# Optimization experiments

Measured on AMD Instinct MI355X. Metric: run time of the kernel, lower is better.

## Reference

```python
import jax, jax.numpy as jnp
import numpy as np

NDIM = 1024
NHEAD = 16
B, T = 4, 2048
EPS = 1e-05
GELU_C = np.sqrt(2.0 / np.pi).astype(np.float32)


def new_gelu(x):
    return 0.5 * x * (1.0 + jnp.tanh(GELU_C * (x + 0.044715 * x ** 3)))


def layer_norm(x, w, b):
    mu = jnp.mean(x, axis=-1, keepdims=True)
    var = jnp.var(x, axis=-1, keepdims=True)
    return (x - mu) * jax.lax.rsqrt(var + EPS) * w + b


def setup_inputs() -> dict:
    key = jax.random.key(0)
    ks = jax.random.split(key, 8)
    d, dff = NDIM, 4 * NDIM
    s = 0.02
    return {
        "x": jax.random.normal(ks[0], (B, T, d), jnp.float32),
        "ln1_w": jnp.ones((d,), jnp.float32),
        "ln1_b": jnp.zeros((d,), jnp.float32),
        "w_attn": jax.random.normal(ks[1], (d, 3 * d), jnp.float32) * s,
        "b_attn": jnp.zeros((3 * d,), jnp.float32),
        "w_proj": jax.random.normal(ks[2], (d, d), jnp.float32) * s,
        "b_proj": jnp.zeros((d,), jnp.float32),
        "ln2_w": jnp.ones((d,), jnp.float32),
        "ln2_b": jnp.zeros((d,), jnp.float32),
        "w_fc": jax.random.normal(ks[3], (d, dff), jnp.float32) * s,
        "b_fc": jnp.zeros((dff,), jnp.float32),
        "w_fc2": jax.random.normal(ks[4], (dff, d), jnp.float32) * s,
        "b_fc2": jnp.zeros((d,), jnp.float32),
    }


def reference(x, ln1_w, ln1_b, w_attn, b_attn, w_proj, b_proj,
              ln2_w, ln2_b, w_fc, b_fc, w_fc2, b_fc2):
    Bx, Tx, C = x.shape
    hd = C // NHEAD
    # --- attention ---
    h = layer_norm(x, ln1_w, ln1_b)
    qkv = h @ w_attn + b_attn                       # [B,T,3C]
    q, k, v = jnp.split(qkv, 3, axis=-1)
    q = q.reshape(Bx, Tx, NHEAD, hd).transpose(0, 2, 1, 3)  # [B,H,T,hd]
    k = k.reshape(Bx, Tx, NHEAD, hd).transpose(0, 2, 1, 3)
    v = v.reshape(Bx, Tx, NHEAD, hd).transpose(0, 2, 1, 3)
    att = jnp.einsum('bhqd,bhkd->bhqk', q, k) * (1.0 / np.sqrt(hd).astype(np.float32))
    causal = jnp.tril(jnp.ones((Tx, Tx), bool))
    att = jnp.where(causal[None, None], att, jnp.float32(-jnp.inf))
    att = jax.nn.softmax(att, axis=-1)
    y = jnp.einsum('bhqk,bhkd->bhqd', att, v)
    y = y.transpose(0, 2, 1, 3).reshape(Bx, Tx, C)
    x = x + y @ w_proj + b_proj
    # --- MLP ---
    h2 = layer_norm(x, ln2_w, ln2_b)
    x = x + new_gelu(h2 @ w_fc + b_fc) @ w_fc2 + b_fc2
    return x
```

## Files before the change

kernel.cpp:

```cpp
#include <hip/hip_runtime.h>

typedef __attribute__((ext_vector_type(8))) short short8;
typedef __attribute__((ext_vector_type(8))) unsigned short ushort8;
typedef __attribute__((ext_vector_type(4))) float f32x4;
typedef __attribute__((ext_vector_type(16))) float f32x16;
typedef __attribute__((ext_vector_type(2))) unsigned int uint2v;
typedef unsigned int uint32;

__device__ __forceinline__ unsigned short f2bf(float f){
  union { float f; unsigned int u; } x; x.f = f;
  unsigned int u = x.u;
  u += 0x7fffu + ((u >> 16) & 1u);
  return (unsigned short)(u >> 16);
}
__device__ __forceinline__ float bf2f(unsigned short s){
  union { float f; unsigned int u; } x; x.u = ((uint32)s) << 16; return x.f;
}

typedef __attribute__((address_space(1))) void gvoid;
typedef __attribute__((address_space(3))) void lvoid;
__device__ __forceinline__ void gload_lds16(const void* g, void* l){
  __builtin_amdgcn_global_load_lds((gvoid*)g, (lvoid*)l, 16, 0, 0);
}

__device__ __forceinline__ f32x4 mfma_bf16(short8 a, short8 b, f32x4 c){
  return __builtin_amdgcn_mfma_f32_16x16x32_bf16(a, b, c, 0, 0, 0);
}
__device__ __forceinline__ f32x16 mfma32(short8 a, short8 b, f32x16 c){
  return __builtin_amdgcn_mfma_f32_32x32x16_bf16(a, b, c, 0, 0, 0);
}

__device__ __forceinline__ uint32 cvtpk_bf(float lo, float hi){
  uint32 r;
  asm("v_cvt_pk_bf16_f32 %0, %1, %2" : "=v"(r) : "v"(lo), "v"(hi));
  return r;
}
__device__ __forceinline__ void plswap(uint32& a, uint32& b){
  auto r = __builtin_amdgcn_permlane32_swap(a, b, false, false);
  a = r[0]; b = r[1];
}

#if __has_builtin(__builtin_amdgcn_exp2f)
__device__ __forceinline__ float exp2g(float x){ return __builtin_amdgcn_exp2f(x); }
#else
__device__ __forceinline__ float exp2g(float x){ return exp2f(x); }
#endif
#if __has_builtin(__builtin_amdgcn_rcpf)
__device__ __forceinline__ float rcpg(float x){ return __builtin_amdgcn_rcpf(x); }
#else
__device__ __forceinline__ float rcpg(float x){ return 1.0f / x; }
#endif

__device__ __forceinline__ float gelu_fast(float v){
  const float u = 0.7978845608028654f * (v + 0.044715f * v * v * v);
  const float E = exp2g(2.8853900817779268f * u);
  return v - v * rcpg(1.0f + E);
}

__device__ __forceinline__ f32x16 zero16(){
  f32x16 z;
  #pragma unroll
  for (int i = 0; i < 16; i++) z[i] = 0.0f;
  return z;
}

__global__ __launch_bounds__(256) void wtrans_all_kernel(
    const float* __restrict__ w0, unsigned short* __restrict__ t0,
    const float* __restrict__ w1, unsigned short* __restrict__ t1,
    const float* __restrict__ w2, unsigned short* __restrict__ t2,
    const float* __restrict__ w3, unsigned short* __restrict__ t3)
{
  __shared__ float tile[32][33];
  const int bt = blockIdx.x;
  const float* w; unsigned short* wt; int K, N, ti;
  if (bt < 3072)      { w = w0; wt = t0; K = 1024; N = 3072; ti = bt; }
  else if (bt < 4096) { w = w1; wt = t1; K = 1024; N = 1024; ti = bt - 3072; }
  else if (bt < 8192) { w = w2; wt = t2; K = 1024; N = 4096; ti = bt - 4096; }
  else                { w = w3; wt = t3; K = 4096; N = 1024; ti = bt - 8192; }
  const int nbx = N >> 5;
  const int n0 = (ti % nbx) << 5;
  const int k0 = (ti / nbx) << 5;
  const int t = threadIdx.x;
  #pragma unroll
  for (int i = 0; i < 4; i++){
    const int e = t + i * 256;
    const int r = e >> 5, c = e & 31;
    tile[r][c] = w[(size_t)(k0 + r) * N + n0 + c];
  }
  __syncthreads();
  #pragma unroll
  for (int i = 0; i < 4; i++){
    const int e = t + i * 256;
    const int r = e >> 5, c = e & 31;
    wt[(size_t)(n0 + r) * K + k0 + c] = f2bf(tile[c][r]);
  }
}

__global__ __launch_bounds__(256) void vtrans_kernel(
    const unsigned short* __restrict__ qkv, unsigned short* __restrict__ vt)
{
  __shared__ unsigned short tile[32][33];
  const int bh = blockIdx.z;
  const int b = bh >> 4, h = bh & 15;
  const int t0 = blockIdx.x * 32;
  const int f0 = blockIdx.y * 32;
  const int t = threadIdx.x;
  #pragma unroll
  for (int i = 0; i < 4; i++){
    const int e = t + i * 256;
    const int r = e >> 5, c = e & 31;
    tile[r][c] = qkv[(size_t)(b * 2048 + t0 + r) * 3072 + 2048 + h * 64 + f0 + c];
  }
  __syncthreads();
  #pragma unroll
  for (int i = 0; i < 4; i++){
    const int e = t + i * 256;
    const int r = e >> 5, c = e & 31;
    vt[((size_t)bh * 64 + f0 + r) * 2048 + t0 + c] = tile[c][r];
  }
}

__global__ __launch_bounds__(256) void ln_kernel(
    const float* __restrict__ x, const float* __restrict__ w, const float* __restrict__ b,
    unsigned short* __restrict__ out)
{
  const int row = blockIdx.x;
  const int t = threadIdx.x;
  const float4 v = ((const float4*)(x + (size_t)row * 1024))[t];
  float s  = v.x + v.y + v.z + v.w;
  float s2 = v.x * v.x + v.y * v.y + v.z * v.z + v.w * v.w;
  #pragma unroll
  for (int off = 32; off > 0; off >>= 1){
    s  += __shfl_xor(s, off);
    s2 += __shfl_xor(s2, off);
  }
  __shared__ float ps[8];
  const int wid = t >> 6;
  if ((t & 63) == 0){ ps[wid] = s; ps[4 + wid] = s2; }
  __syncthreads();
  s  = ps[0] + ps[1] + ps[2] + ps[3];
  s2 = ps[4] + ps[5] + ps[6] + ps[7];
  const float mu  = s * (1.0f / 1024.0f);
  const float var = s2 * (1.0f / 1024.0f) - mu * mu;
  const float rs  = rsqrtf(var + 1e-5f);
  const float4 wv = ((const float4*)w)[t];
  const float4 bv = ((const float4*)b)[t];
  ushort4 ov;
  ov.x = f2bf((v.x - mu) * rs * wv.x + bv.x);
  ov.y = f2bf((v.y - mu) * rs * wv.y + bv.y);
  ov.z = f2bf((v.z - mu) * rs * wv.z + bv.z);
  ov.w = f2bf((v.w - mu) * rs * wv.w + bv.w);
  ((ushort4*)(out + (size_t)row * 1024))[t] = ov;
}

__global__ __launch_bounds__(256) void ln_bf16_kernel(
    const unsigned short* __restrict__ x, const float* __restrict__ w,
    const float* __restrict__ b, unsigned short* __restrict__ out)
{
  const int row = blockIdx.x;
  const int t = threadIdx.x;
  const ushort4 raw = ((const ushort4*)(x + (size_t)row * 1024))[t];
  const float v0 = bf2f(raw.x), v1 = bf2f(raw.y), v2 = bf2f(raw.z), v3 = bf2f(raw.w);
  float s  = v0 + v1 + v2 + v3;
  float s2 = v0 * v0 + v1 * v1 + v2 * v2 + v3 * v3;
  #pragma unroll
  for (int off = 32; off > 0; off >>= 1){
    s  += __shfl_xor(s, off);
    s2 += __shfl_xor(s2, off);
  }
  __shared__ float ps[8];
  const int wid = t >> 6;
  if ((t & 63) == 0){ ps[wid] = s; ps[4 + wid] = s2; }
  __syncthreads();
  s  = ps[0] + ps[1] + ps[2] + ps[3];
  s2 = ps[4] + ps[5] + ps[6] + ps[7];
  const float mu  = s * (1.0f / 1024.0f);
  const float var = s2 * (1.0f / 1024.0f) - mu * mu;
  const float rs  = rsqrtf(var + 1e-5f);
  const float4 wv = ((const float4*)w)[t];
  const float4 bv = ((const float4*)b)[t];
  ushort4 ov;
  ov.x = f2bf((v0 - mu) * rs * wv.x + bv.x);
  ov.y = f2bf((v1 - mu) * rs * wv.y + bv.y);
  ov.z = f2bf((v2 - mu) * rs * wv.z + bv.z);
  ov.w = f2bf((v3 - mu) * rs * wv.w + bv.w);
  ((ushort4*)(out + (size_t)row * 1024))[t] = ov;
}

#define EPI_BF16        0
#define EPI_GELU        1
#define EPI_RESF_OBF    2
#define EPI_RESBF_OF32  3

template<int EPI>
__device__ __forceinline__ void epi_store(void* outp, const void* res,
                                          size_t idx, float v){
  if (EPI == EPI_RESF_OBF){
    ((unsigned short*)outp)[idx] = f2bf(v + ((const float*)res)[idx]);
  } else if (EPI == EPI_RESBF_OF32){
    ((float*)outp)[idx] = v + bf2f(((const unsigned short*)res)[idx]);
  } else if (EPI == EPI_GELU){
    ((unsigned short*)outp)[idx] = f2bf(gelu_fast(v));
  } else {
    ((unsigned short*)outp)[idx] = f2bf(v);
  }
}

template<int EPI>
__global__ __launch_bounds__(256, 2) void gemm5_kernel(
    const unsigned short* __restrict__ A,
    const unsigned short* __restrict__ BT,
    const float* __restrict__ bias,
    const void* __restrict__ res,
    void* __restrict__ outp,
    int M, int N, int K)
{
  constexpr int SLOT = 24576;
  __shared__ __align__(16) char lds[3 * SLOT];

  const int nwg = gridDim.x;
  const int bid = blockIdx.x;
  const int wg = (bid & 7) * (nwg >> 3) + (bid >> 3);
  const int NT = N >> 8;
  const int mt = wg / NT;
  const int nti = wg - mt * NT;
  const int m0 = mt << 7;
  const int n0 = nti << 8;

  const int tid = threadIdx.x;
  const int lane = tid & 63;
  const int wid = tid >> 6;
  const int fr = lane & 15;
  const int fg = lane >> 4;

  const unsigned short* aSrc[2]; int aDst[2];
  #pragma unroll
  for (int l = 0; l < 2; l++){
    const int s = l * 256 + tid;
    const int r = s >> 2, c = s & 3;
    aSrc[l] = A + (size_t)(m0 + r) * K + ((c ^ ((r >> 1) & 3)) << 3);
    aDst[l] = s * 16;
  }
  const unsigned short* bSrc[4]; int bDst[4];
  #pragma unroll
  for (int l = 0; l < 4; l++){
    const int s = l * 256 + tid;
    const int r = s >> 2, c = s & 3;
    bSrc[l] = BT + (size_t)(n0 + r) * K + ((c ^ ((r >> 1) & 3)) << 3);
    bDst[l] = 8192 + s * 16;
  }

  int aOff[8], bOff[4];
  #pragma unroll
  for (int mi = 0; mi < 8; mi++){
    const int row = mi * 16 + fr;
    aOff[mi] = row * 64 + ((fg ^ ((row >> 1) & 3)) << 4);
  }
  #pragma unroll
  for (int nj = 0; nj < 4; nj++){
    const int row = wid * 64 + nj * 16 + fr;
    bOff[nj] = 8192 + row * 64 + ((fg ^ ((row >> 1) & 3)) << 4);
  }

  f32x4 acc[8][4];
  #pragma unroll
  for (int i = 0; i < 8; i++)
    #pragma unroll
    for (int j = 0; j < 4; j++) acc[i][j] = (f32x4){0.f, 0.f, 0.f, 0.f};

#define STAGE5(sl, slot) do { \
    gload_lds16(aSrc[0] + (size_t)(sl) * 32, lds + (slot) + aDst[0]); \
    gload_lds16(aSrc[1] + (size_t)(sl) * 32, lds + (slot) + aDst[1]); \
    gload_lds16(bSrc[0] + (size_t)(sl) * 32, lds + (slot) + bDst[0]); \
    gload_lds16(bSrc[1] + (size_t)(sl) * 32, lds + (slot) + bDst[1]); \
    gload_lds16(bSrc[2] + (size_t)(sl) * 32, lds + (slot) + bDst[2]); \
    gload_lds16(bSrc[3] + (size_t)(sl) * 32, lds + (slot) + bDst[3]); \
  } while (0)

  const int NS = K >> 5;

  STAGE5(0, 0);
  STAGE5(1, SLOT);
  asm volatile("s_waitcnt vmcnt(6)" ::: "memory");
  __builtin_amdgcn_s_barrier();
  asm volatile("" ::: "memory");

  int cs = 0, cg = 2 * SLOT;
  for (int s = 0; s < NS; s++){
    short8 aF[8], bF[4];
    #pragma unroll
    for (int mi = 0; mi < 8; mi++)
      aF[mi] = *(const short8*)(lds + cs + aOff[mi]);
    #pragma unroll
    for (int nj = 0; nj < 4; nj++)
      bF[nj] = *(const short8*)(lds + cs + bOff[nj]);
    if (s + 2 < NS) STAGE5(s + 2, cg);
    #pragma unroll
    for (int mi = 0; mi < 8; mi++)
      #pragma unroll
      for (int nj = 0; nj < 4; nj++)
        acc[mi][nj] = mfma_bf16(aF[mi], bF[nj], acc[mi][nj]);

    if (s + 2 < NS){
      asm volatile("s_waitcnt vmcnt(6)" ::: "memory");
    } else if (s + 1 < NS){
      asm volatile("s_waitcnt vmcnt(0)" ::: "memory");
    }
    __builtin_amdgcn_s_barrier();
    asm volatile("" ::: "memory");

    cs += SLOT; if (cs == 3 * SLOT) cs = 0;
    cg += SLOT; if (cg == 3 * SLOT) cg = 0;
  }
#undef STAGE5

  #pragma unroll
  for (int mi = 0; mi < 8; mi++){
    const int mrow = m0 + mi * 16 + fg * 4;
    #pragma unroll
    for (int nj = 0; nj < 4; nj++){
      const int ncol = n0 + wid * 64 + nj * 16 + fr;
      const float bv = bias[ncol];
      #pragma unroll
      for (int r2 = 0; r2 < 4; r2++){
        const size_t idx = (size_t)(mrow + r2) * N + ncol;
        epi_store<EPI>(outp, res, idx, acc[mi][nj][r2] + bv);
      }
    }
  }
}

template<int EPI>
__global__ __launch_bounds__(256, 3) void gemm7_kernel(
    const unsigned short* __restrict__ A,
    const unsigned short* __restrict__ BT,
    const float* __restrict__ bias,
    const void* __restrict__ res,
    void* __restrict__ outp,
    int M, int N, int K)
{
  constexpr int SLOT = 16384;
  __shared__ __align__(16) char lds[3 * SLOT];

  const int nwg = gridDim.x;
  const int bid = blockIdx.x;
  const int wg = (bid & 7) * (nwg >> 3) + (bid >> 3);
  const int NT = N >> 7;
  const int mt = wg / NT;
  const int nti = wg - mt * NT;
  const int m0 = mt << 7;
  const int n0 = nti << 7;

  const int tid = threadIdx.x;
  const int lane = tid & 63;
  const int wid = tid >> 6;
  const int wv_m = wid >> 1;
  const int wv_n = wid & 1;
  const int fr = lane & 15;
  const int fg = lane >> 4;

  const unsigned short* aSrc[2]; int aDst[2];
  const unsigned short* bSrc[2]; int bDst[2];
  #pragma unroll
  for (int l = 0; l < 2; l++){
    const int s = l * 256 + tid;
    const int r = s >> 2, c = s & 3;
    const int co = (c ^ ((r >> 1) & 3)) << 3;
    aSrc[l] = A  + (size_t)(m0 + r) * K + co;
    bSrc[l] = BT + (size_t)(n0 + r) * K + co;
    aDst[l] = s * 16;
    bDst[l] = 8192 + s * 16;
  }

  int aOff[4], bOff[4];
  #pragma unroll
  for (int mi = 0; mi < 4; mi++){
    const int row = wv_m * 64 + mi * 16 + fr;
    aOff[mi] = row * 64 + ((fg ^ ((row >> 1) & 3)) << 4);
  }
  #pragma unroll
  for (int nj = 0; nj < 4; nj++){
    const int row = wv_n * 64 + nj * 16 + fr;
    bOff[nj] = 8192 + row * 64 + ((fg ^ ((row >> 1) & 3)) << 4);
  }

  f32x4 acc[4][4];
  #pragma unroll
  for (int i = 0; i < 4; i++)
    #pragma unroll
    for (int j = 0; j < 4; j++) acc[i][j] = (f32x4){0.f, 0.f, 0.f, 0.f};

#define STAGE7(sl, slot) do { \
    gload_lds16(aSrc[0] + (size_t)(sl) * 32, lds + (slot) + aDst[0]); \
    gload_lds16(aSrc[1] + (size_t)(sl) * 32, lds + (slot) + aDst[1]); \
    gload_lds16(bSrc[0] + (size_t)(sl) * 32, lds + (slot) + bDst[0]); \
    gload_lds16(bSrc[1] + (size_t)(sl) * 32, lds + (slot) + bDst[1]); \
  } while (0)

  const int NS = K >> 5;

  STAGE7(0, 0);
  STAGE7(1, SLOT);
  asm volatile("s_waitcnt vmcnt(4)" ::: "memory");
  __builtin_amdgcn_s_barrier();
  asm volatile("" ::: "memory");

  int cs = 0, cg = 2 * SLOT;
  for (int s = 0; s < NS; s++){
    short8 aF[4], bF[4];
    #pragma unroll
    for (int mi = 0; mi < 4; mi++)
      aF[mi] = *(const short8*)(lds + cs + aOff[mi]);
    #pragma unroll
    for (int nj = 0; nj < 4; nj++)
      bF[nj] = *(const short8*)(lds + cs + bOff[nj]);
    if (s + 2 < NS) STAGE7(s + 2, cg);
    #pragma unroll
    for (int mi = 0; mi < 4; mi++)
      #pragma unroll
      for (int nj = 0; nj < 4; nj++)
        acc[mi][nj] = mfma_bf16(aF[mi], bF[nj], acc[mi][nj]);

    if (s + 2 < NS){
      asm volatile("s_waitcnt vmcnt(4)" ::: "memory");
    } else if (s + 1 < NS){
      asm volatile("s_waitcnt vmcnt(0)" ::: "memory");
    }
    __builtin_amdgcn_s_barrier();
    asm volatile("" ::: "memory");

    cs += SLOT; if (cs == 3 * SLOT) cs = 0;
    cg += SLOT; if (cg == 3 * SLOT) cg = 0;
  }
#undef STAGE7

  #pragma unroll
  for (int mi = 0; mi < 4; mi++){
    const int mrow = m0 + wv_m * 64 + mi * 16 + fg * 4;
    #pragma unroll
    for (int nj = 0; nj < 4; nj++){
      const int ncol = n0 + wv_n * 64 + nj * 16 + fr;
      const float bv = bias[ncol];
      #pragma unroll
      for (int r2 = 0; r2 < 4; r2++){
        const size_t idx = (size_t)(mrow + r2) * N + ncol;
        epi_store<EPI>(outp, res, idx, acc[mi][nj][r2] + bv);
      }
    }
  }
}

template<bool MASK>
__device__ __forceinline__ void attn_tile(
    const unsigned short* __restrict__ Kc, const unsigned short* __restrict__ Vc,
    const short8 (&qf)[4], int kvbase, int qg, int l31, int hi,
    float& m_r, float& lsum, f32x16& Oa, f32x16& Ob)
{
  f32x16 Sa = zero16();
  f32x16 Sb = zero16();
  const int xb = l31 & 7;
  #pragma unroll
  for (int kk = 0; kk < 4; kk++){
    const int x = kk * 2 + hi;
    const short8 k0 = *(const short8*)((const char*)Kc + l31 * 128 + ((x ^ xb) << 4));
    const short8 k1 = *(const short8*)((const char*)Kc + (l31 + 32) * 128 + ((x ^ xb) << 4));
    Sa = mfma32(k0, qf[kk], Sa);
    Sb = mfma32(k1, qf[kk], Sb);
  }
  if (MASK){
    #pragma unroll
    for (int r = 0; r < 16; r++){
      const int kva = kvbase + (r & 3) + 8 * (r >> 2) + 4 * hi;
      Sa[r] = (kva > qg)      ? -1e30f : Sa[r];
      Sb[r] = (kva + 32 > qg) ? -1e30f : Sb[r];
    }
  }
  float tmax = Sa[0];
  #pragma unroll
  for (int r = 1; r < 16; r++) tmax = fmaxf(tmax, Sa[r]);
  #pragma unroll
  for (int r = 0; r < 16; r++) tmax = fmaxf(tmax, Sb[r]);
  tmax = fmaxf(tmax, __shfl_xor(tmax, 32));
  if (__any(tmax > m_r + 10.0f)){
    const float mn = fmaxf(m_r, tmax);
    const float sc = exp2g(m_r - mn);
    m_r = mn;
    lsum *= sc;
    #pragma unroll
    for (int r = 0; r < 16; r++){ Oa[r] *= sc; Ob[r] *= sc; }
  }
  float rs = 0.0f;
  #pragma unroll
  for (int r = 0; r < 16; r++){
    Sa[r] = exp2g(Sa[r] - m_r); rs += Sa[r];
    Sb[r] = exp2g(Sb[r] - m_r); rs += Sb[r];
  }
  rs += __shfl_xor(rs, 32);
  lsum += rs;

  short8 pf[4];
  {
    uint32 a0 = cvtpk_bf(Sa[0], Sa[1]),   b0 = cvtpk_bf(Sa[4], Sa[5]);
    uint32 a1 = cvtpk_bf(Sa[2], Sa[3]),   b1 = cvtpk_bf(Sa[6], Sa[7]);
    plswap(a0, b0); plswap(a1, b1);
    uint32 a2 = cvtpk_bf(Sa[8], Sa[9]),   b2 = cvtpk_bf(Sa[12], Sa[13]);
    uint32 a3 = cvtpk_bf(Sa[10], Sa[11]), b3 = cvtpk_bf(Sa[14], Sa[15]);
    plswap(a2, b2); plswap(a3, b3);
    union { uint32 u[4]; short8 s; } m0, m1;
    m0.u[0] = a0; m0.u[1] = a1; m0.u[2] = b0; m0.u[3] = b1;
    m1.u[0] = a2; m1.u[1] = a3; m1.u[2] = b2; m1.u[3] = b3;
    pf[0] = m0.s; pf[1] = m1.s;
  }
  {
    uint32 a0 = cvtpk_bf(Sb[0], Sb[1]),   b0 = cvtpk_bf(Sb[4], Sb[5]);
    uint32 a1 = cvtpk_bf(Sb[2], Sb[3]),   b1 = cvtpk_bf(Sb[6], Sb[7]);
    plswap(a0, b0); plswap(a1, b1);
    uint32 a2 = cvtpk_bf(Sb[8], Sb[9]),   b2 = cvtpk_bf(Sb[12], Sb[13]);
    uint32 a3 = cvtpk_bf(Sb[10], Sb[11]), b3 = cvtpk_bf(Sb[14], Sb[15]);
    plswap(a2, b2); plswap(a3, b3);
    union { uint32 u[4]; short8 s; } m0, m1;
    m0.u[0] = a0; m0.u[1] = a1; m0.u[2] = b0; m0.u[3] = b1;
    m1.u[0] = a2; m1.u[1] = a3; m1.u[2] = b2; m1.u[3] = b3;
    pf[2] = m0.s; pf[3] = m1.s;
  }
  #pragma unroll
  for (int kk = 0; kk < 4; kk++){
    const int x = kk * 2 + hi;
    const short8 v0 = *(const short8*)((const char*)Vc + l31 * 128 + ((x ^ xb) << 4));
    const short8 v1 = *(const short8*)((const char*)Vc + (l31 + 32) * 128 + ((x ^ xb) << 4));
    Oa = mfma32(v0, pf[kk], Oa);
    Ob = mfma32(v1, pf[kk], Ob);
  }
}

__global__ __launch_bounds__(256) void attn_kernel(
    const unsigned short* __restrict__ qkv,
    const unsigned short* __restrict__ vt,
    unsigned short* __restrict__ y)
{
  __shared__ __align__(16) unsigned short Klds[2][4096];
  __shared__ __align__(16) unsigned short Vlds[2][4096];
  const int bid = blockIdx.x;
  const int bh = bid & 63;
  const int qb_i = 15 - (bid >> 6);
  const int b = bh >> 4, h = bh & 15;
  const int qb0 = qb_i * 128;
  const int tid = threadIdx.x;
  const int w = tid >> 6;
  const int lane = tid & 63;
  const int l31 = lane & 31;
  const int hi = lane >> 5;

  const int qrow_g = b * 2048 + qb0 + w * 32 + l31;
  const unsigned short* qp = qkv + (size_t)qrow_g * 3072 + h * 64;
  short8 qf[4];
  #pragma unroll
  for (int kk = 0; kk < 4; kk++){
    short8 raw = *(const short8*)&qp[kk * 16 + hi * 8];
    #pragma unroll
    for (int j = 0; j < 8; j++)
      qf[kk][j] = (short)f2bf(bf2f((unsigned short)raw[j]) * 0.18033688011112042f);
  }

  const int sr = tid >> 3;
  const int ce = ((tid & 7) ^ (sr & 7)) * 8;
  const unsigned short* kb = qkv + (size_t)(b * 2048) * 3072 + 1024 + h * 64;
  const unsigned short* vb = vt + (size_t)bh * 64 * 2048;

  f32x16 Oa = zero16(), Ob = zero16();
  float m_r = -1e30f, lsum = 0.0f;
  const int qmin = qb0 + w * 32;
  const int qmax = qmin + 31;
  const int qg = qmin + l31;
  const int nkv = (qb0 >> 6) + 2;

#define STAGE(t, bb) do { \
    const size_t kro = (size_t)((t) * 64 + sr) * 3072; \
    gload_lds16(kb + kro + ce,                         (char*)&Klds[bb][0] + tid * 16); \
    gload_lds16(kb + kro + (size_t)32 * 3072 + ce,     (char*)&Klds[bb][0] + 4096 + tid * 16); \
    gload_lds16(vb + (size_t)sr * 2048 + (t) * 64 + ce,        (char*)&Vlds[bb][0] + tid * 16); \
    gload_lds16(vb + (size_t)(sr + 32) * 2048 + (t) * 64 + ce, (char*)&Vlds[bb][0] + 4096 + tid * 16); \
  } while (0)

  STAGE(0, 0);
  __syncthreads();
  int cur = 0;
  for (int kvt = 0; kvt < nkv; kvt++){
    if (kvt + 1 < nkv){
      if (cur) STAGE(kvt + 1, 0); else STAGE(kvt + 1, 1);
    }
    if (kvt * 64 <= qmax){
      if (kvt * 64 + 63 <= qmin)
        attn_tile<false>(Klds[cur], Vlds[cur], qf, kvt * 64, qg, l31, hi, m_r, lsum, Oa, Ob);
      else
        attn_tile<true >(Klds[cur], Vlds[cur], qf, kvt * 64, qg, l31, hi, m_r, lsum, Oa, Ob);
    }
    __syncthreads();
    cur ^= 1;
  }
#undef STAGE

  const float inv = 1.0f / lsum;
  unsigned short* yp = y + (size_t)qrow_g * 1024 + h * 64;
  #pragma unroll
  for (int c2 = 0; c2 < 4; c2++){
    uint2v da, db;
    da.x = cvtpk_bf(Oa[4 * c2 + 0] * inv, Oa[4 * c2 + 1] * inv);
    da.y = cvtpk_bf(Oa[4 * c2 + 2] * inv, Oa[4 * c2 + 3] * inv);
    *(uint2v*)&yp[8 * c2 + 4 * hi] = da;
    db.x = cvtpk_bf(Ob[4 * c2 + 0] * inv, Ob[4 * c2 + 1] * inv);
    db.y = cvtpk_bf(Ob[4 * c2 + 2] * inv, Ob[4 * c2 + 3] * inv);
    *(uint2v*)&yp[32 + 8 * c2 + 4 * hi] = db;
  }
}

extern "C" void kernel_launch(void* const* d_in, const int* in_sizes, int n_in,
                              void* d_out, int out_size, void* d_ws, size_t ws_size,
                              hipStream_t stream)
{
  const float* x      = (const float*)d_in[0];
  const float* ln1_w  = (const float*)d_in[1];
  const float* ln1_b  = (const float*)d_in[2];
  const float* w_attn = (const float*)d_in[3];
  const float* b_attn = (const float*)d_in[4];
  const float* w_proj = (const float*)d_in[5];
  const float* b_proj = (const float*)d_in[6];
  const float* ln2_w  = (const float*)d_in[7];
  const float* ln2_b  = (const float*)d_in[8];
  const float* w_fc   = (const float*)d_in[9];
  const float* b_fc   = (const float*)d_in[10];
  const float* w_fc2  = (const float*)d_in[11];
  const float* b_fc2  = (const float*)d_in[12];

  char* ws = (char*)d_ws;
  unsigned short* wbT_attn = (unsigned short*)(ws + 0);
  unsigned short* wbT_proj = (unsigned short*)(ws + 6291456);
  unsigned short* wbT_fc   = (unsigned short*)(ws + 8388608);
  unsigned short* wbT_fc2  = (unsigned short*)(ws + 16777216);
  unsigned short* h_bf     = (unsigned short*)(ws + 25165824);
  unsigned short* qkv_bf   = (unsigned short*)(ws + 41943040);
  unsigned short* vt_bf    = (unsigned short*)(ws + 92274688);
  unsigned short* g_bf     = (unsigned short*)(ws + 41943040);
  unsigned short* y_bf     = (unsigned short*)(ws + 109051904);
  unsigned short* x1_bf    = (unsigned short*)(ws + 125829120);
  float* outf = (float*)d_out;

  wtrans_all_kernel<<<12288, 256, 0, stream>>>(
      w_attn, wbT_attn, w_proj, wbT_proj, w_fc, wbT_fc, w_fc2, wbT_fc2);

  ln_kernel<<<8192, 256, 0, stream>>>(x, ln1_w, ln1_b, h_bf);
  gemm5_kernel<EPI_BF16><<<768, 256, 0, stream>>>(
      h_bf, wbT_attn, b_attn, nullptr, qkv_bf, 8192, 3072, 1024);
  vtrans_kernel<<<dim3(64, 2, 64), 256, 0, stream>>>(qkv_bf, vt_bf);
  attn_kernel<<<1024, 256, 0, stream>>>(qkv_bf, vt_bf, y_bf);
  gemm7_kernel<EPI_RESF_OBF><<<512, 256, 0, stream>>>(
      y_bf, wbT_proj, b_proj, x, x1_bf, 8192, 1024, 1024);
  ln_bf16_kernel<<<8192, 256, 0, stream>>>(x1_bf, ln2_w, ln2_b, h_bf);
  gemm5_kernel<EPI_GELU><<<1024, 256, 0, stream>>>(
      h_bf, wbT_fc, b_fc, nullptr, g_bf, 8192, 4096, 1024);
  gemm7_kernel<EPI_RESBF_OF32><<<512, 256, 0, stream>>>(
      g_bf, wbT_fc2, b_fc2, x1_bf, outf, 8192, 1024, 4096);
}
```

Baseline: 343.8 us.

## Split-K the fc2 GEMM with 128x256 tiles and a separate reduction kernel

The final fc2 GEMM (K=4096) now runs on the larger 128x256 gemm5 tile path with K split into two halves. Each half writes a bf16 partial into reused scratch buffers (h_bf, y_bf). A new row-wise kernel then sums the two partials, adds the bias and the x1 residual, and writes fp32 output. The aim is more work per workgroup and better tile efficiency while keeping 512 workgroups in flight. In exchange it adds an extra kernel launch, extra global traffic for the partials, and precision loss from rounding the partials to bf16.

```diff
diff --git a/kernel.cpp b/kernel.cpp
--- a/kernel.cpp
+++ b/kernel.cpp
@@ -187,10 +187,31 @@
   ((ushort4*)(out + (size_t)row * 1024))[t] = ov;
 }
 
+__global__ __launch_bounds__(256) void skred_kernel(
+    const unsigned short* __restrict__ p0, const unsigned short* __restrict__ p1,
+    const float* __restrict__ bias, const unsigned short* __restrict__ x1,
+    float* __restrict__ out)
+{
+  const int row = blockIdx.x;
+  const int t = threadIdx.x;
+  const size_t base = (size_t)row * 1024 + t * 4;
+  const ushort4 a = *(const ushort4*)(p0 + base);
+  const ushort4 b = *(const ushort4*)(p1 + base);
+  const ushort4 c = *(const ushort4*)(x1 + base);
+  const float4 bv = ((const float4*)bias)[t];
+  float4 o;
+  o.x = bf2f(a.x) + bf2f(b.x) + bv.x + bf2f(c.x);
+  o.y = bf2f(a.y) + bf2f(b.y) + bv.y + bf2f(c.y);
+  o.z = bf2f(a.z) + bf2f(b.z) + bv.z + bf2f(c.z);
+  o.w = bf2f(a.w) + bf2f(b.w) + bv.w + bf2f(c.w);
+  *(float4*)(out + base) = o;
+}
+
 #define EPI_BF16        0
 #define EPI_GELU        1
 #define EPI_RESF_OBF    2
 #define EPI_RESBF_OF32  3
+#define EPI_PARTBF      4
 
 template<int EPI>
 __device__ __forceinline__ void epi_store(void* outp, const void* res,
@@ -207,25 +228,15 @@
 }
 
 template<int EPI>
-__global__ __launch_bounds__(256, 2) void gemm5_kernel(
+__device__ __forceinline__ void gemm5_core(
     const unsigned short* __restrict__ A,
     const unsigned short* __restrict__ BT,
     const float* __restrict__ bias,
     const void* __restrict__ res,
     void* __restrict__ outp,
-    int M, int N, int K)
+    int N, int K, int Ks, int m0, int n0, char* lds)
 {
   constexpr int SLOT = 24576;
-  __shared__ __align__(16) char lds[3 * SLOT];
-
-  const int nwg = gridDim.x;
-  const int bid = blockIdx.x;
-  const int wg = (bid & 7) * (nwg >> 3) + (bid >> 3);
-  const int NT = N >> 8;
-  const int mt = wg / NT;
-  const int nti = wg - mt * NT;
-  const int m0 = mt << 7;
-  const int n0 = nti << 8;
 
   const int tid = threadIdx.x;
   const int lane = tid & 63;
@@ -238,7 +249,7 @@
   for (int l = 0; l < 2; l++){
     const int s = l * 256 + tid;
     const int r = s >> 2, c = s & 3;
-    aSrc[l] = A + (size_t)(m0 + r) * K + ((c ^ ((r >> 1) & 3)) << 3);
+    aSrc[l] = A + (size_t)(m0 + r) * Ks + ((c ^ ((r >> 1) & 3)) << 3);
     aDst[l] = s * 16;
   }
   const unsigned short* bSrc[4]; int bDst[4];
@@ -246,7 +257,7 @@
   for (int l = 0; l < 4; l++){
     const int s = l * 256 + tid;
     const int r = s >> 2, c = s & 3;
-    bSrc[l] = BT + (size_t)(n0 + r) * K + ((c ^ ((r >> 1) & 3)) << 3);
+    bSrc[l] = BT + (size_t)(n0 + r) * Ks + ((c ^ ((r >> 1) & 3)) << 3);
     bDst[l] = 8192 + s * 16;
   }
 
@@ -320,7 +331,7 @@
     #pragma unroll
     for (int nj = 0; nj < 4; nj++){
       const int ncol = n0 + wid * 64 + nj * 16 + fr;
-      const float bv = bias[ncol];
+      const float bv = (EPI == EPI_PARTBF) ? 0.0f : bias[ncol];
       #pragma unroll
       for (int r2 = 0; r2 < 4; r2++){
         const size_t idx = (size_t)(mrow + r2) * N + ncol;
@@ -328,6 +339,48 @@
       }
     }
   }
+}
+
+template<int EPI>
+__global__ __launch_bounds__(256, 2) void gemm5_kernel(
+    const unsigned short* __restrict__ A,
+    const unsigned short* __restrict__ BT,
+    const float* __restrict__ bias,
+    const void* __restrict__ res,
+    void* __restrict__ outp,
+    int M, int N, int K)
+{
+  __shared__ __align__(16) char lds[3 * 24576];
+  const int nwg = gridDim.x;
+  const int bid = blockIdx.x;
+  const int wg = (bid & 7) * (nwg >> 3) + (bid >> 3);
+  const int NT = N >> 8;
+  const int mt = wg / NT;
+  const int nti = wg - mt * NT;
+  gemm5_core<EPI>(A, BT, bias, res, outp, N, K, K, mt << 7, nti << 8, lds);
+}
+
+__global__ __launch_bounds__(256, 2) void gemm5sk_kernel(
+    const unsigned short* __restrict__ A,
+    const unsigned short* __restrict__ BT,
+    unsigned short* __restrict__ p0,
+    unsigned short* __restrict__ p1,
+    int N, int Khalf, int Ks)
+{
+  __shared__ __align__(16) char lds[3 * 24576];
+  const int nwg = gridDim.x;
+  const int bid = blockIdx.x;
+  const int wg = (bid & 7) * (nwg >> 3) + (bid >> 3);
+  const int half = wg & 1;
+  const int tile = wg >> 1;
+  const int NT = N >> 8;
+  const int mt = tile / NT;
+  const int nti = tile - mt * NT;
+  const unsigned short* Ae = A + (size_t)half * Khalf;
+  const unsigned short* Be = BT + (size_t)half * Khalf;
+  unsigned short* pe = half ? p1 : p0;
+  gemm5_core<EPI_PARTBF>(Ae, Be, nullptr, nullptr, pe, N, Khalf, Ks,
+                         mt << 7, nti << 8, lds);
 }
 
 template<int EPI>
@@ -658,6 +711,7 @@
   ln_bf16_kernel<<<8192, 256, 0, stream>>>(x1_bf, ln2_w, ln2_b, h_bf);
   gemm5_kernel<EPI_GELU><<<1024, 256, 0, stream>>>(
       h_bf, wbT_fc, b_fc, nullptr, g_bf, 8192, 4096, 1024);
-  gemm7_kernel<EPI_RESBF_OF32><<<512, 256, 0, stream>>>(
-      g_bf, wbT_fc2, b_fc2, x1_bf, outf, 8192, 1024, 4096);
-}
+  gemm5sk_kernel<<<512, 256, 0, stream>>>(
+      g_bf, wbT_fc2, h_bf, y_bf, 1024, 2048, 4096);
+  skred_kernel<<<8192, 256, 0, stream>>>(h_bf, y_bf, b_fc2, x1_bf, outf);
+}
```

Measured after the change: 352.0 us. 2.4% more time.
